# Kernel optimization log

Measured on AMD Instinct MI355X. Metric: run time of the kernel, lower is better.

## Reference

```python
import jax, jax.numpy as jnp
import numpy as np

H = 12        # num heads
DH = 64       # head dim
W = 8         # window size
WIN2 = W * W  # tokens per window


def _relative_position_index():
    # Swin-style relative position index, [WIN2, WIN2] int array (static).
    coords = np.stack(np.meshgrid(np.arange(W), np.arange(W), indexing='ij'))  # [2,W,W]
    flat = coords.reshape(2, -1)                                               # [2,WIN2]
    rel = flat[:, :, None] - flat[:, None, :]                                  # [2,WIN2,WIN2]
    rel = rel.transpose(1, 2, 0).astype(np.int64)
    rel[..., 0] += W - 1
    rel[..., 1] += W - 1
    rel[..., 0] *= 2 * W - 1
    return rel.sum(-1)  # [WIN2, WIN2]


def setup_inputs() -> dict:
    key = jax.random.key(0)
    ks = jax.random.split(key, 12)
    B, S, D = 128, 256, 768
    scale = 0.02
    return {
        'q': jax.random.normal(ks[0], (B, S, D), jnp.float32),
        'k': jax.random.normal(ks[1], (B, S, D), jnp.float32),
        'v': jax.random.normal(ks[2], (B, S, D), jnp.float32),
        'Wq': jax.random.normal(ks[3], (D, D), jnp.float32) * scale,
        'bq': jnp.zeros((D,), jnp.float32),
        'Wk': jax.random.normal(ks[4], (D, D), jnp.float32) * scale,
        'bk': jnp.zeros((D,), jnp.float32),
        'Wv': jax.random.normal(ks[5], (D, D), jnp.float32) * scale,
        'bv': jnp.zeros((D,), jnp.float32),
        'Wo': jax.random.normal(ks[6], (D, D), jnp.float32) * scale,
        'bo': jnp.zeros((D,), jnp.float32),
        'bias_table': jax.random.normal(ks[7], ((2 * W - 1) ** 2, H), jnp.float32) * scale,
    }


def reference(q, k, v, Wq, bq, Wk, bk, Wv, bv, Wo, bo, bias_table):
    B, S, D = q.shape

    def proj(x, Wt, bt):
        # Linear stores weight as [out, in]; y = x @ W^T + b, then split heads.
        return (x @ Wt.T + bt).reshape(B, S, H, DH).transpose(0, 2, 1, 3)

    qh = proj(q, Wq, bq)  # [B,H,S,DH]
    kh = proj(k, Wk, bk)
    vh = proj(v, Wv, bv)

    scores = jnp.einsum('bhqd,bhkd->bhqk', qh, kh) / np.float32(np.sqrt(DH))

    idx = _relative_position_index()                         # static [WIN2,WIN2]
    bias = bias_table[idx.reshape(-1)].reshape(WIN2, WIN2, H)
    bias = bias.transpose(2, 0, 1)                           # [H,WIN2,WIN2]
    n_contrast = S // WIN2
    bias = jnp.tile(bias, (1, n_contrast, n_contrast))       # [H,S,S]

    probs = jax.nn.softmax(scores + bias[None], axis=-1)     # dropout p=0 (eval)
    ctx = jnp.einsum('bhqk,bhkd->bhqd', probs, vh)
    ctx = ctx.transpose(0, 2, 1, 3).reshape(B, S, D)
    return ctx @ Wo.T + bo
```

## Files before the change

kernel.cpp:

```cpp
#include <hip/hip_runtime.h>


typedef __bf16 bf16;
typedef __bf16 bf16x8 __attribute__((ext_vector_type(8)));
typedef float  f32x4  __attribute__((ext_vector_type(4)));

#define MFMA_BF16(a, b, c) __builtin_amdgcn_mfma_f32_16x16x32_bf16((a), (b), (c), 0, 0, 0)

__device__ __forceinline__ void gld16(const void* g, void* l) {
    __builtin_amdgcn_global_load_lds(
        (const __attribute__((address_space(1))) void*)g,
        (__attribute__((address_space(3))) void*)l, 16, 0, 0);
}

__device__ __forceinline__ bf16x8 pack8(f32x4 lo, f32x4 hi) {
    bf16x8 r;
    r[0] = (bf16)lo[0]; r[1] = (bf16)lo[1]; r[2] = (bf16)lo[2]; r[3] = (bf16)lo[3];
    r[4] = (bf16)hi[0]; r[5] = (bf16)hi[1]; r[6] = (bf16)hi[2]; r[7] = (bf16)hi[3];
    return r;
}

__device__ __forceinline__ int swz8(int row, int g) { return g ^ (row & 7); }

__global__ __launch_bounds__(256)
void gemm_qkv(const float* __restrict__ q, const float* __restrict__ k,
              const float* __restrict__ v,
              const float* __restrict__ Wq, const float* __restrict__ Wk,
              const float* __restrict__ Wv,
              const float* __restrict__ bq, const float* __restrict__ bk,
              const float* __restrict__ bv, bf16* __restrict__ outbase)
{
    __shared__ bf16 As[2][128 * 64];
    __shared__ bf16 Bs[2][128 * 64];

    const int z = blockIdx.z;
    const float* X    = (z == 0) ? q  : (z == 1) ? k  : v;
    const float* Wt   = (z == 0) ? Wq : (z == 1) ? Wk : Wv;
    const float* bias = (z == 0) ? bq : (z == 1) ? bk : bv;
    bf16* out = outbase + (size_t)z * 25165824;

    const int tid  = threadIdx.x;
    const int m0   = blockIdx.x * 128;
    const int n0   = blockIdx.y * 128;
    const int w    = tid >> 6;
    const int lane = tid & 63;
    const int quad = lane >> 4;
    const int l15  = lane & 15;
    const int wr   = (w >> 1) * 64;
    const int wc   = (w & 1) * 64;

    int srow[4], sgp[4], sdst[4];
    #pragma unroll
    for (int p = 0; p < 4; ++p) {
        int g = p * 256 + tid;
        srow[p] = g >> 3;
        sgp[p]  = g & 7;
        sdst[p] = srow[p] * 64 + swz8(srow[p], sgp[p]) * 8;
    }

    f32x4 acc[4][4] = {};
    f32x4 aL[4], aH[4], bL[4], bH[4];

    auto load_stage = [&](int k0) {
        #pragma unroll
        for (int p = 0; p < 4; ++p) {
            const float* sa = X + (size_t)(m0 + srow[p]) * 768 + k0 + sgp[p] * 8;
            aL[p] = *(const f32x4*)sa;
            aH[p] = *(const f32x4*)(sa + 4);
            const float* sb = Wt + (size_t)(n0 + srow[p]) * 768 + k0 + sgp[p] * 8;
            bL[p] = *(const f32x4*)sb;
            bH[p] = *(const f32x4*)(sb + 4);
        }
    };
    auto write_stage = [&](int buf) {
        #pragma unroll
        for (int p = 0; p < 4; ++p) {
            *(bf16x8*)&As[buf][sdst[p]] = pack8(aL[p], aH[p]);
            *(bf16x8*)&Bs[buf][sdst[p]] = pack8(bL[p], bH[p]);
        }
    };
    auto compute = [&](int buf) {
        #pragma unroll
        for (int kk = 0; kk < 2; ++kk) {
            bf16x8 af[4], bfr[4];
            #pragma unroll
            for (int mt = 0; mt < 4; ++mt) {
                int row = wr + mt * 16 + l15;
                af[mt] = *(const bf16x8*)&As[buf][row * 64 + swz8(row, kk * 4 + quad) * 8];
            }
            #pragma unroll
            for (int nt = 0; nt < 4; ++nt) {
                int row = wc + nt * 16 + l15;
                bfr[nt] = *(const bf16x8*)&Bs[buf][row * 64 + swz8(row, kk * 4 + quad) * 8];
            }
            #pragma unroll
            for (int mt = 0; mt < 4; ++mt)
                #pragma unroll
                for (int nt = 0; nt < 4; ++nt)
                    acc[mt][nt] = MFMA_BF16(af[mt], bfr[nt], acc[mt][nt]);
        }
    };

    load_stage(0);
    write_stage(0);
    __syncthreads();

    int cur = 0;
    for (int kt = 0; kt < 11; ++kt) {
        load_stage((kt + 1) * 64);
        compute(cur);
        write_stage(cur ^ 1);
        __syncthreads();
        cur ^= 1;
    }
    compute(cur);

    #pragma unroll
    for (int mt = 0; mt < 4; ++mt) {
        #pragma unroll
        for (int nt = 0; nt < 4; ++nt) {
            int gn = n0 + wc + nt * 16 + l15;
            float bv = bias[gn];
            int h = gn >> 6, d = gn & 63;
            #pragma unroll
            for (int r = 0; r < 4; ++r) {
                int gm = m0 + wr + mt * 16 + quad * 4 + r;
                int b = gm >> 8, s = gm & 255;
                out[(((size_t)(b * 12 + h) << 8) + s) * 64 + d] = (bf16)(acc[mt][nt][r] + bv);
            }
        }
    }
}

__global__ __launch_bounds__(256)
void gemm_out(const bf16* __restrict__ X, const float* __restrict__ Wt,
              const float* __restrict__ bias, float* __restrict__ out)
{
    __shared__ bf16 As[2][128 * 64];
    __shared__ bf16 Bs[2][128 * 64];

    const int tid  = threadIdx.x;
    const int m0   = blockIdx.x * 128;
    const int n0   = blockIdx.y * 128;
    const int w    = tid >> 6;
    const int lane = tid & 63;
    const int quad = lane >> 4;
    const int l15  = lane & 15;
    const int wr   = (w >> 1) * 64;
    const int wc   = (w & 1) * 64;

    int srow[4], sgp[4], sdst[4];
    #pragma unroll
    for (int p = 0; p < 4; ++p) {
        int g = p * 256 + tid;
        srow[p] = g >> 3;
        sgp[p]  = g & 7;
        sdst[p] = srow[p] * 64 + swz8(srow[p], sgp[p]) * 8;
    }

    f32x4 acc[4][4] = {};
    bf16x8 aR[4];
    f32x4 bL[4], bH[4];

    auto load_stage = [&](int k0) {
        #pragma unroll
        for (int p = 0; p < 4; ++p) {
            aR[p] = *(const bf16x8*)(X + (size_t)(m0 + srow[p]) * 768 + k0 + sgp[p] * 8);
            const float* sb = Wt + (size_t)(n0 + srow[p]) * 768 + k0 + sgp[p] * 8;
            bL[p] = *(const f32x4*)sb;
            bH[p] = *(const f32x4*)(sb + 4);
        }
    };
    auto write_stage = [&](int buf) {
        #pragma unroll
        for (int p = 0; p < 4; ++p) {
            *(bf16x8*)&As[buf][sdst[p]] = aR[p];
            *(bf16x8*)&Bs[buf][sdst[p]] = pack8(bL[p], bH[p]);
        }
    };
    auto compute = [&](int buf) {
        #pragma unroll
        for (int kk = 0; kk < 2; ++kk) {
            bf16x8 af[4], bfr[4];
            #pragma unroll
            for (int mt = 0; mt < 4; ++mt) {
                int row = wr + mt * 16 + l15;
                af[mt] = *(const bf16x8*)&As[buf][row * 64 + swz8(row, kk * 4 + quad) * 8];
            }
            #pragma unroll
            for (int nt = 0; nt < 4; ++nt) {
                int row = wc + nt * 16 + l15;
                bfr[nt] = *(const bf16x8*)&Bs[buf][row * 64 + swz8(row, kk * 4 + quad) * 8];
            }
            #pragma unroll
            for (int mt = 0; mt < 4; ++mt)
                #pragma unroll
                for (int nt = 0; nt < 4; ++nt)
                    acc[mt][nt] = MFMA_BF16(af[mt], bfr[nt], acc[mt][nt]);
        }
    };

    load_stage(0);
    write_stage(0);
    __syncthreads();

    int cur = 0;
    for (int kt = 0; kt < 11; ++kt) {
        load_stage((kt + 1) * 64);
        compute(cur);
        write_stage(cur ^ 1);
        __syncthreads();
        cur ^= 1;
    }
    compute(cur);

    #pragma unroll
    for (int mt = 0; mt < 4; ++mt) {
        #pragma unroll
        for (int nt = 0; nt < 4; ++nt) {
            int gn = n0 + wc + nt * 16 + l15;
            float bv = bias[gn];
            #pragma unroll
            for (int r = 0; r < 4; ++r) {
                int gm = m0 + wr + mt * 16 + quad * 4 + r;
                out[(size_t)gm * 768 + gn] = acc[mt][nt][r] + bv;
            }
        }
    }
}

__global__ __launch_bounds__(256)
void transpose_v(const bf16* __restrict__ vh, bf16* __restrict__ vt)
{
    __shared__ bf16 Ts[64 * 65];
    const int qt = blockIdx.x, h = blockIdx.y, b = blockIdx.z;
    const bf16* src = vh + ((size_t)(b * 12 + h) * 256 + qt * 64) * 64;
    bf16* dst = vt + (size_t)(b * 12 + h) * 64 * 256;

    const int tid = threadIdx.x;
    {
        int row = tid >> 2, c0 = (tid & 3) * 16;
        bf16x8 v0 = *(const bf16x8*)(src + row * 64 + c0);
        bf16x8 v1 = *(const bf16x8*)(src + row * 64 + c0 + 8);
        #pragma unroll
        for (int i = 0; i < 8; ++i) {
            Ts[row * 65 + c0 + i]     = v0[i];
            Ts[row * 65 + c0 + 8 + i] = v1[i];
        }
    }
    __syncthreads();
    {
        int d = tid >> 2, j0 = (tid & 3) * 16;
        bf16x8 o0, o1;
        #pragma unroll
        for (int i = 0; i < 8; ++i) {
            o0[i] = Ts[(j0 + i) * 65 + d];
            o1[i] = Ts[(j0 + 8 + i) * 65 + d];
        }
        *(bf16x8*)(dst + (size_t)d * 256 + qt * 64 + j0)     = o0;
        *(bf16x8*)(dst + (size_t)d * 256 + qt * 64 + j0 + 8) = o1;
    }
}

__global__ __launch_bounds__(256)
void attn_kernel(const bf16* __restrict__ qh, const bf16* __restrict__ kh,
                 const bf16* __restrict__ vt, const float* __restrict__ table,
                 bf16* __restrict__ ctx)
{
    __shared__ bf16 Qs[64 * 64];
    __shared__ bf16 Ks[64 * 64];
    __shared__ bf16 Vs[64 * 64];
    __shared__ bf16 Ps[4 * 16 * 72];
    __shared__ bf16 Bsh[64 * 68];

    const int tid  = threadIdx.x;
    const int qt   = blockIdx.x;
    const int h    = blockIdx.y;
    const int b    = blockIdx.z;
    const int w    = tid >> 6;
    const int lane = tid & 63;
    const int quad = lane >> 4;
    const int l15  = lane & 15;

    const size_t bh = (size_t)(b * 12 + h) * 256 * 64;
    const bf16* Qg  = qh + bh + (size_t)qt * 64 * 64;
    const bf16* Kg  = kh + bh;
    const bf16* Vtg = vt + bh;

    #pragma unroll
    for (int p = 0; p < 2; ++p) {
        int g = p * 256 + tid;
        gld16(Qg + (size_t)(g >> 3) * 64 + (g & 7) * 8, (char*)Qs + g * 16);
    }
    {
        int i = tid >> 2, j0 = (tid & 3) * 16;
        int ai = i >> 3, aj = i & 7;
        #pragma unroll
        for (int jj = 0; jj < 16; ++jj) {
            int j = j0 + jj;
            int idx = (ai - (j >> 3) + 7) * 15 + (aj - (j & 7) + 7);
            Bsh[i * 68 + j] = (bf16)table[idx * 12 + h];
        }
    }

    f32x4 sacc[16] = {};
    bf16x8 qf0, qf1;
    for (int c = 0; c < 4; ++c) {
        __syncthreads();
        #pragma unroll
        for (int p = 0; p < 2; ++p) {
            int g = p * 256 + tid;
            gld16(Kg + (size_t)(c * 64 + (g >> 3)) * 64 + (g & 7) * 8, (char*)Ks + g * 16);
        }
        __syncthreads();
        if (c == 0) {
            qf0 = *(const bf16x8*)&Qs[(w * 16 + l15) * 64 + quad * 8];
            qf1 = *(const bf16x8*)&Qs[(w * 16 + l15) * 64 + 32 + quad * 8];
        }
        #pragma unroll
        for (int jtl = 0; jtl < 4; ++jtl) {
            bf16x8 kf0 = *(const bf16x8*)&Ks[(jtl * 16 + l15) * 64 + quad * 8];
            bf16x8 kf1 = *(const bf16x8*)&Ks[(jtl * 16 + l15) * 64 + 32 + quad * 8];
            sacc[c * 4 + jtl] = MFMA_BF16(qf0, kf0, sacc[c * 4 + jtl]);
            sacc[c * 4 + jtl] = MFMA_BF16(qf1, kf1, sacc[c * 4 + jtl]);
        }
    }

    const int browbase = w * 16 + quad * 4;
    float p[16][4];
    #pragma unroll
    for (int jt = 0; jt < 16; ++jt) {
        int jcol = ((jt * 16) & 63) + l15;
        #pragma unroll
        for (int r = 0; r < 4; ++r)
            p[jt][r] = sacc[jt][r] * 0.125f + (float)Bsh[(browbase + r) * 68 + jcol];
    }
    float invl[4];
    #pragma unroll
    for (int r = 0; r < 4; ++r) {
        float m = p[0][r];
        #pragma unroll
        for (int jt = 1; jt < 16; ++jt) m = fmaxf(m, p[jt][r]);
        #pragma unroll
        for (int off = 1; off < 16; off <<= 1)
            m = fmaxf(m, __shfl_xor(m, off, 64));
        float s = 0.f;
        #pragma unroll
        for (int jt = 0; jt < 16; ++jt) {
            p[jt][r] = __expf(p[jt][r] - m);
            s += p[jt][r];
        }
        #pragma unroll
        for (int off = 1; off < 16; off <<= 1)
            s += __shfl_xor(s, off, 64);
        invl[r] = 1.0f / s;
    }

    f32x4 cacc[4] = {};
    bf16* Pw = &Ps[w * 16 * 72];
    for (int c = 0; c < 4; ++c) {
        __syncthreads();
        #pragma unroll
        for (int pp = 0; pp < 2; ++pp) {
            int g = pp * 256 + tid;
            gld16(Vtg + (size_t)(g >> 3) * 256 + c * 64 + (g & 7) * 8, (char*)Vs + g * 16);
        }
        #pragma unroll
        for (int jtl = 0; jtl < 4; ++jtl) {
            int jt = c * 4 + jtl;
            #pragma unroll
            for (int r = 0; r < 4; ++r)
                Pw[(quad * 4 + r) * 72 + jtl * 16 + l15] = (bf16)(p[jt][r] * invl[r]);
        }
        __syncthreads();
        bf16x8 pf0 = *(const bf16x8*)&Pw[l15 * 72 + quad * 8];
        bf16x8 pf1 = *(const bf16x8*)&Pw[l15 * 72 + 32 + quad * 8];
        #pragma unroll
        for (int dt = 0; dt < 4; ++dt) {
            bf16x8 vf0 = *(const bf16x8*)&Vs[(dt * 16 + l15) * 64 + quad * 8];
            bf16x8 vf1 = *(const bf16x8*)&Vs[(dt * 16 + l15) * 64 + 32 + quad * 8];
            cacc[dt] = MFMA_BF16(pf0, vf0, cacc[dt]);
            cacc[dt] = MFMA_BF16(pf1, vf1, cacc[dt]);
        }
    }

    const size_t obase = ((size_t)b * 256) * 768 + (size_t)h * 64;
    #pragma unroll
    for (int dt = 0; dt < 4; ++dt) {
        #pragma unroll
        for (int r = 0; r < 4; ++r) {
            int s = qt * 64 + w * 16 + quad * 4 + r;
            int d = dt * 16 + l15;
            ctx[obase + (size_t)s * 768 + d] = (bf16)cacc[dt][r];
        }
    }
}

extern "C" void kernel_launch(void* const* d_in, const int* in_sizes, int n_in,
                              void* d_out, int out_size, void* d_ws, size_t ws_size,
                              hipStream_t stream) {
    (void)in_sizes; (void)n_in; (void)out_size; (void)ws_size;
    const float* q     = (const float*)d_in[0];
    const float* k     = (const float*)d_in[1];
    const float* v     = (const float*)d_in[2];
    const float* Wq    = (const float*)d_in[3];
    const float* bq    = (const float*)d_in[4];
    const float* Wk    = (const float*)d_in[5];
    const float* bk    = (const float*)d_in[6];
    const float* Wv    = (const float*)d_in[7];
    const float* bv    = (const float*)d_in[8];
    const float* Wo    = (const float*)d_in[9];
    const float* bo    = (const float*)d_in[10];
    const float* table = (const float*)d_in[11];

    const size_t NE = (size_t)128 * 256 * 768;
    bf16* qh  = (bf16*)d_ws;
    bf16* kh  = qh + NE;
    bf16* vh  = kh + NE;
    bf16* vt  = vh + NE;
    bf16* ctx = vh;
    float* out = (float*)d_out;

    dim3 blk(256);
    gemm_qkv<<<dim3(256, 6, 3), blk, 0, stream>>>(q, k, v, Wq, Wk, Wv, bq, bk, bv, qh);
    transpose_v<<<dim3(4, 12, 128), blk, 0, stream>>>(vh, vt);
    attn_kernel<<<dim3(4, 12, 128), blk, 0, stream>>>(qh, kh, vt, table, ctx);
    gemm_out<<<dim3(256, 6), blk, 0, stream>>>(ctx, Wo, bo, out);
}
```

Measured before the change: 739.2 us.

## Pre-convert inputs and weights to bf16, use direct global-to-LDS loads in GEMMs

Adds a conversion kernel that turns the fp32 activations and weights into bf16 in scratch space (the output buffer and workspace regions that are free at that point). The QKV and output GEMMs then stage tiles with global_load_lds straight into swizzled shared memory, which removes the register round trip and the in-loop packing. The GEMM tiles are also remapped with a grouped block order to improve L2 reuse. The cost is an extra read and write pass over the inputs and more kernel launches, and the schedule depends on carefully ordered reuse of the aliased buffers.

```diff
diff --git a/kernel.cpp b/kernel.cpp
--- a/kernel.cpp
+++ b/kernel.cpp
@@ -23,25 +23,31 @@
 __device__ __forceinline__ int swz8(int row, int g) { return g ^ (row & 7); }
 
 __global__ __launch_bounds__(256)
-void gemm_qkv(const float* __restrict__ q, const float* __restrict__ k,
-              const float* __restrict__ v,
-              const float* __restrict__ Wq, const float* __restrict__ Wk,
-              const float* __restrict__ Wv,
-              const float* __restrict__ bq, const float* __restrict__ bk,
-              const float* __restrict__ bv, bf16* __restrict__ outbase)
+void cvt_f32_bf16(const float* __restrict__ src, bf16* __restrict__ dst, int ngroups)
+{
+    int i = blockIdx.x * 256 + threadIdx.x;
+    const int stride = gridDim.x * 256;
+    for (; i < ngroups; i += stride) {
+        const f32x4* s = (const f32x4*)(src + (size_t)i * 8);
+        *(bf16x8*)(dst + (size_t)i * 8) = pack8(s[0], s[1]);
+    }
+}
+
+__global__ __launch_bounds__(256)
+void gemm_qkv_b(const bf16* __restrict__ X, const bf16* __restrict__ Wb,
+                const float* __restrict__ bias, bf16* __restrict__ out)
 {
     __shared__ bf16 As[2][128 * 64];
     __shared__ bf16 Bs[2][128 * 64];
 
-    const int z = blockIdx.z;
-    const float* X    = (z == 0) ? q  : (z == 1) ? k  : v;
-    const float* Wt   = (z == 0) ? Wq : (z == 1) ? Wk : Wv;
-    const float* bias = (z == 0) ? bq : (z == 1) ? bk : bv;
-    bf16* out = outbase + (size_t)z * 25165824;
+    const int wg  = blockIdx.x;
+    const int pos = wg >> 3;
+    const int mi  = (wg & 7) * 32 + pos / 6;
+    const int ni  = pos % 6;
+    const int m0  = mi * 128;
+    const int n0  = ni * 128;
 
     const int tid  = threadIdx.x;
-    const int m0   = blockIdx.x * 128;
-    const int n0   = blockIdx.y * 128;
     const int w    = tid >> 6;
     const int lane = tid & 63;
     const int quad = lane >> 4;
@@ -49,34 +55,16 @@
     const int wr   = (w >> 1) * 64;
     const int wc   = (w & 1) * 64;
 
-    int srow[4], sgp[4], sdst[4];
-    #pragma unroll
-    for (int p = 0; p < 4; ++p) {
-        int g = p * 256 + tid;
-        srow[p] = g >> 3;
-        sgp[p]  = g & 7;
-        sdst[p] = srow[p] * 64 + swz8(srow[p], sgp[p]) * 8;
-    }
-
     f32x4 acc[4][4] = {};
-    f32x4 aL[4], aH[4], bL[4], bH[4];
-
-    auto load_stage = [&](int k0) {
+
+    auto stage = [&](int buf, int k0) {
         #pragma unroll
         for (int p = 0; p < 4; ++p) {
-            const float* sa = X + (size_t)(m0 + srow[p]) * 768 + k0 + sgp[p] * 8;
-            aL[p] = *(const f32x4*)sa;
-            aH[p] = *(const f32x4*)(sa + 4);
-            const float* sb = Wt + (size_t)(n0 + srow[p]) * 768 + k0 + sgp[p] * 8;
-            bL[p] = *(const f32x4*)sb;
-            bH[p] = *(const f32x4*)(sb + 4);
-        }
-    };
-    auto write_stage = [&](int buf) {
-        #pragma unroll
-        for (int p = 0; p < 4; ++p) {
-            *(bf16x8*)&As[buf][sdst[p]] = pack8(aL[p], aH[p]);
-            *(bf16x8*)&Bs[buf][sdst[p]] = pack8(bL[p], bH[p]);
+            int g = p * 256 + tid;
+            int row = g >> 3, slot = g & 7;
+            int cg  = slot ^ (row & 7);
+            gld16(X  + (size_t)(m0 + row) * 768 + k0 + cg * 8, (char*)&As[buf][0] + g * 16);
+            gld16(Wb + (size_t)(n0 + row) * 768 + k0 + cg * 8, (char*)&Bs[buf][0] + g * 16);
         }
     };
     auto compute = [&](int buf) {
@@ -101,15 +89,12 @@
         }
     };
 
-    load_stage(0);
-    write_stage(0);
+    stage(0, 0);
     __syncthreads();
-
     int cur = 0;
     for (int kt = 0; kt < 11; ++kt) {
-        load_stage((kt + 1) * 64);
+        stage(cur ^ 1, (kt + 1) * 64);
         compute(cur);
-        write_stage(cur ^ 1);
         __syncthreads();
         cur ^= 1;
     }
@@ -133,15 +118,20 @@
 }
 
 __global__ __launch_bounds__(256)
-void gemm_out(const bf16* __restrict__ X, const float* __restrict__ Wt,
-              const float* __restrict__ bias, float* __restrict__ out)
+void gemm_out_b(const bf16* __restrict__ X, const bf16* __restrict__ Wb,
+                const float* __restrict__ bias, float* __restrict__ out)
 {
     __shared__ bf16 As[2][128 * 64];
     __shared__ bf16 Bs[2][128 * 64];
 
+    const int wg  = blockIdx.x;
+    const int pos = wg >> 3;
+    const int mi  = (wg & 7) * 32 + pos / 6;
+    const int ni  = pos % 6;
+    const int m0  = mi * 128;
+    const int n0  = ni * 128;
+
     const int tid  = threadIdx.x;
-    const int m0   = blockIdx.x * 128;
-    const int n0   = blockIdx.y * 128;
     const int w    = tid >> 6;
     const int lane = tid & 63;
     const int quad = lane >> 4;
@@ -149,33 +139,16 @@
     const int wr   = (w >> 1) * 64;
     const int wc   = (w & 1) * 64;
 
-    int srow[4], sgp[4], sdst[4];
-    #pragma unroll
-    for (int p = 0; p < 4; ++p) {
-        int g = p * 256 + tid;
-        srow[p] = g >> 3;
-        sgp[p]  = g & 7;
-        sdst[p] = srow[p] * 64 + swz8(srow[p], sgp[p]) * 8;
-    }
-
     f32x4 acc[4][4] = {};
-    bf16x8 aR[4];
-    f32x4 bL[4], bH[4];
-
-    auto load_stage = [&](int k0) {
+
+    auto stage = [&](int buf, int k0) {
         #pragma unroll
         for (int p = 0; p < 4; ++p) {
-            aR[p] = *(const bf16x8*)(X + (size_t)(m0 + srow[p]) * 768 + k0 + sgp[p] * 8);
-            const float* sb = Wt + (size_t)(n0 + srow[p]) * 768 + k0 + sgp[p] * 8;
-            bL[p] = *(const f32x4*)sb;
-            bH[p] = *(const f32x4*)(sb + 4);
-        }
-    };
-    auto write_stage = [&](int buf) {
-        #pragma unroll
-        for (int p = 0; p < 4; ++p) {
-            *(bf16x8*)&As[buf][sdst[p]] = aR[p];
-            *(bf16x8*)&Bs[buf][sdst[p]] = pack8(bL[p], bH[p]);
+            int g = p * 256 + tid;
+            int row = g >> 3, slot = g & 7;
+            int cg  = slot ^ (row & 7);
+            gld16(X  + (size_t)(m0 + row) * 768 + k0 + cg * 8, (char*)&As[buf][0] + g * 16);
+            gld16(Wb + (size_t)(n0 + row) * 768 + k0 + cg * 8, (char*)&Bs[buf][0] + g * 16);
         }
     };
     auto compute = [&](int buf) {
@@ -200,15 +173,12 @@
         }
     };
 
-    load_stage(0);
-    write_stage(0);
+    stage(0, 0);
     __syncthreads();
-
     int cur = 0;
     for (int kt = 0; kt < 11; ++kt) {
-        load_stage((kt + 1) * 64);
+        stage(cur ^ 1, (kt + 1) * 64);
         compute(cur);
-        write_stage(cur ^ 1);
         __syncthreads();
         cur ^= 1;
     }
@@ -414,6 +384,8 @@
     const float* table = (const float*)d_in[11];
 
     const size_t NE = (size_t)128 * 256 * 768;
+    const size_t WE = (size_t)768 * 768;
+
     bf16* qh  = (bf16*)d_ws;
     bf16* kh  = qh + NE;
     bf16* vh  = kh + NE;
@@ -421,9 +393,32 @@
     bf16* ctx = vh;
     float* out = (float*)d_out;
 
+    bf16* xq_b = (bf16*)d_out;
+    bf16* xk_b = xq_b + NE;
+    bf16* xv_b = xq_b;
+    bf16* wq_b = vt;
+    bf16* wk_b = wq_b + WE;
+    bf16* wv_b = wk_b + WE;
+    bf16* wo_b = qh;
+
+    const int XG = (int)(NE / 8);
+    const int WG = (int)(WE / 8);
+
     dim3 blk(256);
-    gemm_qkv<<<dim3(256, 6, 3), blk, 0, stream>>>(q, k, v, Wq, Wk, Wv, bq, bk, bv, qh);
+    cvt_f32_bf16<<<2048, blk, 0, stream>>>(q,  xq_b, XG);
+    cvt_f32_bf16<<<2048, blk, 0, stream>>>(k,  xk_b, XG);
+    cvt_f32_bf16<<<288,  blk, 0, stream>>>(Wq, wq_b, WG);
+    cvt_f32_bf16<<<288,  blk, 0, stream>>>(Wk, wk_b, WG);
+    cvt_f32_bf16<<<288,  blk, 0, stream>>>(Wv, wv_b, WG);
+
+    gemm_qkv_b<<<1536, blk, 0, stream>>>(xq_b, wq_b, bq, qh);
+    gemm_qkv_b<<<1536, blk, 0, stream>>>(xk_b, wk_b, bk, kh);
+    cvt_f32_bf16<<<2048, blk, 0, stream>>>(v, xv_b, XG);
+    gemm_qkv_b<<<1536, blk, 0, stream>>>(xv_b, wv_b, bv, vh);
+
     transpose_v<<<dim3(4, 12, 128), blk, 0, stream>>>(vh, vt);
     attn_kernel<<<dim3(4, 12, 128), blk, 0, stream>>>(qh, kh, vt, table, ctx);
-    gemm_out<<<dim3(256, 6), blk, 0, stream>>>(ctx, Wo, bo, out);
-}
+
+    cvt_f32_bf16<<<288, blk, 0, stream>>>(Wo, wo_b, WG);
+    gemm_out_b<<<1536, blk, 0, stream>>>(ctx, wo_b, bo, out);
+}
```

New measurement: 709.0 us. 1.04x faster.
